# Kernel tuning notes

Hardware: AMD Instinct MI355X
Metric: run time of the kernel (lower is better)

Reference implementation:

```python
import jax, jax.numpy as jnp
import numpy as np

B, N, S, H = 8, 512, 4096, 1024

def setup_inputs() -> dict:
    key = jax.random.key(0)
    k1, k2, k3 = jax.random.split(key, 3)
    doc_state = jax.random.normal(k1, (B, S, H), dtype=jnp.float32)
    # token->node membership mask (soft weights in [0,1), structurally a sparse/binary mask)
    nodes_mapping = jax.random.uniform(k2, (B, N, S), dtype=jnp.float32)
    # node lengths: positive, in [1, S) to avoid divide-by-near-zero
    nodes_len = jax.random.uniform(k3, (B, N), dtype=jnp.float32, minval=1.0, maxval=float(S))
    return {"doc_state": doc_state, "nodes_mapping": nodes_mapping, "nodes_len": nodes_len}

def reference(doc_state, nodes_mapping, nodes_len):
    # Faithful math: sum_s nodes_mapping[b,n,s] * doc_state[b,s,h] / nodes_len[b,n]
    # Expressed as a batched matmul instead of materializing [B,N,S,H].
    pooled = jnp.einsum('bns,bsh->bnh', nodes_mapping, doc_state)
    return pooled / nodes_len[:, :, None]
```

## Files before the change

kernel.cpp:

```cpp
#include <hip/hip_runtime.h>
#include <hip/hip_bf16.h>


typedef __bf16 bf16x8 __attribute__((ext_vector_type(8)));
typedef float  f32x4  __attribute__((ext_vector_type(4)));

#define MFMA16(a, b, c) __builtin_amdgcn_mfma_f32_16x16x32_bf16(a, b, c, 0, 0, 0)

constexpr int Bsz = 8;
constexpr int Nn  = 512;
constexpr int Ss  = 4096;
constexpr int Hh  = 1024;

constexpr int BM = 128, BN = 64, BK = 32;
constexpr int LDK = 40;
constexpr int NT  = Ss / BK;
constexpr int NWG = Bsz * (Nn / BM) * (Hh / BN);

struct StageRegs {
    f32x4 a[4];
    float b[8];
};

__device__ __forceinline__ void issue_loads(StageRegs& r, const float* Ab, const float* Bb,
                                            int s0, int ra, int ka, int hbb, int kb) {
    const float* ap = Ab + (size_t)ra * Ss + s0 + ka;
    #pragma unroll
    for (int i = 0; i < 4; i++) r.a[i] = *(const f32x4*)(ap + i * 4);
    const float* bp = Bb + (size_t)(s0 + kb * 8) * Hh + hbb;
    #pragma unroll
    for (int j = 0; j < 8; j++) r.b[j] = bp[(size_t)j * Hh];
}

__device__ __forceinline__ void write_lds(__bf16* As, __bf16* Bs, const StageRegs& r,
                                          int ra, int ka, int hbb, int kb) {
    bf16x8 v0, v1, w;
    #pragma unroll
    for (int i = 0; i < 8; i++) {
        v0[i] = (__bf16)r.a[i >> 2][i & 3];
        v1[i] = (__bf16)r.a[2 + (i >> 2)][i & 3];
        w[i]  = (__bf16)r.b[i];
    }
    *(bf16x8*)&As[ra * LDK + ka]     = v0;
    *(bf16x8*)&As[ra * LDK + ka + 8] = v1;
    *(bf16x8*)&Bs[hbb * LDK + kb * 8] = w;
}

__device__ __forceinline__ void compute(const __bf16* As, const __bf16* Bs,
                                        f32x4 acc[4][2], int wr, int wc, int l15, int l4) {
    bf16x8 aF[4], bF[2];
    #pragma unroll
    for (int m = 0; m < 4; m++)
        aF[m] = *(const bf16x8*)&As[(wr * 64 + m * 16 + l15) * LDK + l4 * 8];
    #pragma unroll
    for (int n = 0; n < 2; n++)
        bF[n] = *(const bf16x8*)&Bs[(wc * 32 + n * 16 + l15) * LDK + l4 * 8];
    #pragma unroll
    for (int m = 0; m < 4; m++)
        #pragma unroll
        for (int n = 0; n < 2; n++)
            acc[m][n] = MFMA16(aF[m], bF[n], acc[m][n]);
}

__global__ __launch_bounds__(256, 2)
void mean_pool_gemm(const float* __restrict__ doc,
                    const float* __restrict__ map,
                    const float* __restrict__ len,
                    float* __restrict__ out)
{
    __shared__ __align__(16) __bf16 As0[BM * LDK], As1[BM * LDK];
    __shared__ __align__(16) __bf16 Bs0[BN * LDK], Bs1[BN * LDK];

    const int blk = (blockIdx.x & 7) * (NWG / 8) + (blockIdx.x >> 3);
    const int b   = blk >> 6;
    const int rem = blk & 63;
    const int mt  = rem >> 4;
    const int ht  = rem & 15;
    const int n0  = mt * BM;
    const int h0  = ht * BN;

    const int tid  = threadIdx.x;
    const int wave = tid >> 6;
    const int lane = tid & 63;
    const int wr   = wave >> 1;
    const int wc   = wave & 1;
    const int l15  = lane & 15;
    const int l4   = lane >> 4;

    const float* Ab = map + (size_t)b * Nn * Ss + (size_t)n0 * Ss;
    const float* Bb = doc + (size_t)b * Ss * Hh + h0;

    const int ra = tid >> 1;
    const int ka = (tid & 1) * 16;
    const int hbb = tid & 63;
    const int kb  = tid >> 6;

    StageRegs r0, r1;
    f32x4 acc[4][2] = {};

    issue_loads(r0, Ab, Bb, 0,  ra, ka, hbb, kb);
    issue_loads(r1, Ab, Bb, BK, ra, ka, hbb, kb);
    write_lds(As0, Bs0, r0, ra, ka, hbb, kb);
    asm volatile("s_waitcnt lgkmcnt(0)" ::: "memory");
    __builtin_amdgcn_s_barrier();

    for (int t = 0; t < NT; t += 2) {
        {
            const int s2 = (t + 2 < NT ? t + 2 : NT - 1) * BK;
            issue_loads(r0, Ab, Bb, s2, ra, ka, hbb, kb);
            write_lds(As1, Bs1, r1, ra, ka, hbb, kb);
            compute(As0, Bs0, acc, wr, wc, l15, l4);
            asm volatile("s_waitcnt lgkmcnt(0)" ::: "memory");
            __builtin_amdgcn_s_barrier();
        }
        {
            const int s3 = (t + 3 < NT ? t + 3 : NT - 1) * BK;
            issue_loads(r1, Ab, Bb, s3, ra, ka, hbb, kb);
            write_lds(As0, Bs0, r0, ra, ka, hbb, kb);
            compute(As1, Bs1, acc, wr, wc, l15, l4);
            asm volatile("s_waitcnt lgkmcnt(0)" ::: "memory");
            __builtin_amdgcn_s_barrier();
        }
    }

    const float* lenb = len + b * Nn + n0 + wr * 64;
    float* ob = out + (size_t)b * Nn * Hh + (size_t)(n0 + wr * 64) * Hh + h0 + wc * 32;
    #pragma unroll
    for (int m = 0; m < 4; m++) {
        float inv[4];
        #pragma unroll
        for (int j = 0; j < 4; j++) inv[j] = 1.0f / lenb[m * 16 + l4 * 4 + j];
        #pragma unroll
        for (int n = 0; n < 2; n++) {
            #pragma unroll
            for (int j = 0; j < 4; j++) {
                const int row = m * 16 + l4 * 4 + j;
                ob[(size_t)row * Hh + n * 16 + l15] = acc[m][n][j] * inv[j];
            }
        }
    }
}

extern "C" void kernel_launch(void* const* d_in, const int* in_sizes, int n_in,
                              void* d_out, int out_size, void* d_ws, size_t ws_size,
                              hipStream_t stream) {
    const float* doc = (const float*)d_in[0];
    const float* map = (const float*)d_in[1];
    const float* len = (const float*)d_in[2];
    float* out = (float*)d_out;

    dim3 grid(NWG);
    dim3 block(256);
    hipLaunchKernelGGL(mean_pool_gemm, grid, block, 0, stream, doc, map, len, out);
}
```

Baseline: 342.7 us.

## Use 256x256 tiles with split-K over S and atomic accumulation

Grows the output tile to 256x256 with 512-thread blocks and splits the S reduction four ways, so each block loads far less redundant A/B data per output. Partial results are combined with float atomicAdd into an output zeroed by a memset before launch. The double-register prefetch becomes a single-stage register prefetch. This adds atomic traffic, a memset and possible nondeterminism, and the large accumulator array (128 floats per lane) risks register pressure at one block per CU.

```diff
diff --git a/kernel.cpp b/kernel.cpp
--- a/kernel.cpp
+++ b/kernel.cpp
@@ -12,131 +12,126 @@
 constexpr int Ss  = 4096;
 constexpr int Hh  = 1024;
 
-constexpr int BM = 128, BN = 64, BK = 32;
+constexpr int BM = 256, BN = 256, BK = 32;
+constexpr int SPLITK = 4;
+constexpr int KC  = Ss / SPLITK;
+constexpr int NT  = KC / BK;
 constexpr int LDK = 40;
-constexpr int NT  = Ss / BK;
-constexpr int NWG = Bsz * (Nn / BM) * (Hh / BN);
+constexpr int NWG = Bsz * (Nn / BM) * (Hh / BN) * SPLITK;
 
 struct StageRegs {
     f32x4 a[4];
-    float b[8];
+    float b[16];
 };
 
 __device__ __forceinline__ void issue_loads(StageRegs& r, const float* Ab, const float* Bb,
-                                            int s0, int ra, int ka, int hbb, int kb) {
+                                            int s0, int ra, int ka, int hb, int kc) {
     const float* ap = Ab + (size_t)ra * Ss + s0 + ka;
     #pragma unroll
     for (int i = 0; i < 4; i++) r.a[i] = *(const f32x4*)(ap + i * 4);
-    const float* bp = Bb + (size_t)(s0 + kb * 8) * Hh + hbb;
+    const float* bp = Bb + (size_t)(s0 + kc * 16) * Hh + hb;
     #pragma unroll
-    for (int j = 0; j < 8; j++) r.b[j] = bp[(size_t)j * Hh];
+    for (int j = 0; j < 16; j++) r.b[j] = bp[(size_t)j * Hh];
 }
 
 __device__ __forceinline__ void write_lds(__bf16* As, __bf16* Bs, const StageRegs& r,
-                                          int ra, int ka, int hbb, int kb) {
-    bf16x8 v0, v1, w;
+                                          int ra, int ka, int hb, int kc) {
+    bf16x8 v0, v1, w0, w1;
     #pragma unroll
     for (int i = 0; i < 8; i++) {
         v0[i] = (__bf16)r.a[i >> 2][i & 3];
         v1[i] = (__bf16)r.a[2 + (i >> 2)][i & 3];
-        w[i]  = (__bf16)r.b[i];
+        w0[i] = (__bf16)r.b[i];
+        w1[i] = (__bf16)r.b[8 + i];
     }
-    *(bf16x8*)&As[ra * LDK + ka]     = v0;
-    *(bf16x8*)&As[ra * LDK + ka + 8] = v1;
-    *(bf16x8*)&Bs[hbb * LDK + kb * 8] = w;
+    *(bf16x8*)&As[ra * LDK + ka]          = v0;
+    *(bf16x8*)&As[ra * LDK + ka + 8]      = v1;
+    *(bf16x8*)&Bs[hb * LDK + kc * 16]     = w0;
+    *(bf16x8*)&Bs[hb * LDK + kc * 16 + 8] = w1;
 }
 
 __device__ __forceinline__ void compute(const __bf16* As, const __bf16* Bs,
-                                        f32x4 acc[4][2], int wr, int wc, int l15, int l4) {
-    bf16x8 aF[4], bF[2];
+                                        f32x4 acc[8][4], int wr, int wc, int l15, int l4) {
+    bf16x8 aF[8], bF[4];
     #pragma unroll
-    for (int m = 0; m < 4; m++)
-        aF[m] = *(const bf16x8*)&As[(wr * 64 + m * 16 + l15) * LDK + l4 * 8];
+    for (int m = 0; m < 8; m++)
+        aF[m] = *(const bf16x8*)&As[(wr * 128 + m * 16 + l15) * LDK + l4 * 8];
     #pragma unroll
-    for (int n = 0; n < 2; n++)
-        bF[n] = *(const bf16x8*)&Bs[(wc * 32 + n * 16 + l15) * LDK + l4 * 8];
+    for (int n = 0; n < 4; n++)
+        bF[n] = *(const bf16x8*)&Bs[(wc * 64 + n * 16 + l15) * LDK + l4 * 8];
     #pragma unroll
-    for (int m = 0; m < 4; m++)
+    for (int m = 0; m < 8; m++)
         #pragma unroll
-        for (int n = 0; n < 2; n++)
+        for (int n = 0; n < 4; n++)
             acc[m][n] = MFMA16(aF[m], bF[n], acc[m][n]);
 }
 
-__global__ __launch_bounds__(256, 2)
+__global__ __launch_bounds__(512, 1)
 void mean_pool_gemm(const float* __restrict__ doc,
                     const float* __restrict__ map,
                     const float* __restrict__ len,
-                    float* __restrict__ out)
+                    float* out)
 {
-    __shared__ __align__(16) __bf16 As0[BM * LDK], As1[BM * LDK];
-    __shared__ __align__(16) __bf16 Bs0[BN * LDK], Bs1[BN * LDK];
+    __shared__ __align__(16) __bf16 As[2][BM * LDK];
+    __shared__ __align__(16) __bf16 Bs[2][BN * LDK];
 
-    const int blk = (blockIdx.x & 7) * (NWG / 8) + (blockIdx.x >> 3);
-    const int b   = blk >> 6;
-    const int rem = blk & 63;
-    const int mt  = rem >> 4;
-    const int ht  = rem & 15;
-    const int n0  = mt * BM;
-    const int h0  = ht * BN;
+    const int logical = (blockIdx.x & 7) * (NWG / 8) + (blockIdx.x >> 3);
+    const int b  = logical >> 5;
+    const int s  = (logical >> 3) & 3;
+    const int mt = (logical >> 2) & 1;
+    const int ht = logical & 3;
+    const int n0 = mt * BM, h0 = ht * BN, k0 = s * KC;
 
     const int tid  = threadIdx.x;
     const int wave = tid >> 6;
     const int lane = tid & 63;
-    const int wr   = wave >> 1;
-    const int wc   = wave & 1;
+    const int wr   = wave >> 2;
+    const int wc   = wave & 3;
     const int l15  = lane & 15;
     const int l4   = lane >> 4;
 
-    const float* Ab = map + (size_t)b * Nn * Ss + (size_t)n0 * Ss;
-    const float* Bb = doc + (size_t)b * Ss * Hh + h0;
+    const float* Ab = map + (size_t)b * Nn * Ss + (size_t)n0 * Ss + k0;
+    const float* Bb = doc + (size_t)b * Ss * Hh + (size_t)k0 * Hh + h0;
 
     const int ra = tid >> 1;
     const int ka = (tid & 1) * 16;
-    const int hbb = tid & 63;
-    const int kb  = tid >> 6;
+    const int hb = tid >> 1;
+    const int kc = tid & 1;
 
-    StageRegs r0, r1;
-    f32x4 acc[4][2] = {};
+    StageRegs r;
+    f32x4 acc[8][4] = {};
 
-    issue_loads(r0, Ab, Bb, 0,  ra, ka, hbb, kb);
-    issue_loads(r1, Ab, Bb, BK, ra, ka, hbb, kb);
-    write_lds(As0, Bs0, r0, ra, ka, hbb, kb);
+    issue_loads(r, Ab, Bb, 0, ra, ka, hb, kc);
+    write_lds(As[0], Bs[0], r, ra, ka, hb, kc);
     asm volatile("s_waitcnt lgkmcnt(0)" ::: "memory");
     __builtin_amdgcn_s_barrier();
 
-    for (int t = 0; t < NT; t += 2) {
-        {
-            const int s2 = (t + 2 < NT ? t + 2 : NT - 1) * BK;
-            issue_loads(r0, Ab, Bb, s2, ra, ka, hbb, kb);
-            write_lds(As1, Bs1, r1, ra, ka, hbb, kb);
-            compute(As0, Bs0, acc, wr, wc, l15, l4);
+    int cur = 0;
+    for (int t = 0; t < NT; ++t) {
+        if (t + 1 < NT)
+            issue_loads(r, Ab, Bb, (t + 1) * BK, ra, ka, hb, kc);
+        compute(As[cur], Bs[cur], acc, wr, wc, l15, l4);
+        if (t + 1 < NT) {
+            write_lds(As[cur ^ 1], Bs[cur ^ 1], r, ra, ka, hb, kc);
             asm volatile("s_waitcnt lgkmcnt(0)" ::: "memory");
             __builtin_amdgcn_s_barrier();
-        }
-        {
-            const int s3 = (t + 3 < NT ? t + 3 : NT - 1) * BK;
-            issue_loads(r1, Ab, Bb, s3, ra, ka, hbb, kb);
-            write_lds(As0, Bs0, r0, ra, ka, hbb, kb);
-            compute(As1, Bs1, acc, wr, wc, l15, l4);
-            asm volatile("s_waitcnt lgkmcnt(0)" ::: "memory");
-            __builtin_amdgcn_s_barrier();
+            cur ^= 1;
         }
     }
 
-    const float* lenb = len + b * Nn + n0 + wr * 64;
-    float* ob = out + (size_t)b * Nn * Hh + (size_t)(n0 + wr * 64) * Hh + h0 + wc * 32;
+    const float* lenp = len + b * Nn + n0 + wr * 128;
+    float* ob = out + (size_t)b * Nn * Hh + (size_t)(n0 + wr * 128) * Hh + h0 + wc * 64;
     #pragma unroll
-    for (int m = 0; m < 4; m++) {
+    for (int m = 0; m < 8; m++) {
+        const int row_l = m * 16 + l4 * 4;
         float inv[4];
         #pragma unroll
-        for (int j = 0; j < 4; j++) inv[j] = 1.0f / lenb[m * 16 + l4 * 4 + j];
+        for (int j = 0; j < 4; j++) inv[j] = 1.0f / lenp[row_l + j];
         #pragma unroll
-        for (int n = 0; n < 2; n++) {
+        for (int n = 0; n < 4; n++) {
             #pragma unroll
-            for (int j = 0; j < 4; j++) {
-                const int row = m * 16 + l4 * 4 + j;
-                ob[(size_t)row * Hh + n * 16 + l15] = acc[m][n][j] * inv[j];
-            }
+            for (int j = 0; j < 4; j++)
+                atomicAdd(&ob[(size_t)(row_l + j) * Hh + n * 16 + l15], acc[m][n][j] * inv[j]);
         }
     }
 }
@@ -149,7 +144,9 @@
     const float* len = (const float*)d_in[2];
     float* out = (float*)d_out;
 
+    hipMemsetAsync(out, 0, (size_t)out_size * sizeof(float), stream);
+
     dim3 grid(NWG);
-    dim3 block(256);
+    dim3 block(512);
     hipLaunchKernelGGL(mean_pool_gemm, grid, block, 0, stream, doc, map, len, out);
 }
```

Result: faster. 324.7 us (-5.3%).
